# Optimization experiments

Measured on AMD Instinct MI355X. Metric: run time of the kernel, lower is better.

## Reference

```python
import jax, jax.numpy as jnp
import numpy as np

N = 100_000      # nodes
E = 500_000      # edges
D = 128          # node_feature_dim
IN = 2 * D       # VAE in_features
H = 128          # hidden_ch
L = 5            # latent_features
V2 = 3.5
BETA = 10.0


def _init_linear(key, fan_in, fan_out):
    kw, kb = jax.random.split(key)
    bound = 1.0 / np.sqrt(fan_in)
    W = jax.random.uniform(kw, (fan_in, fan_out), jnp.float32, -bound, bound)
    b = jax.random.uniform(kb, (fan_out,), jnp.float32, -bound, bound)
    return W, b


def setup_inputs() -> dict:
    key = jax.random.key(0)
    ks = jax.random.split(key, 12)
    x = jax.random.normal(ks[0], (N, D), jnp.float32)
    row = jax.random.randint(ks[1], (E,), 0, N, jnp.int32)
    col = jax.random.randint(ks[2], (E,), 0, N, jnp.int32)
    eps = jax.random.normal(ks[3], (E, L), jnp.float32)
    # encoder FCBlock: IN -> H -> H -> H -> 2L (ReLU on hidden layers)
    eW0, eb0 = _init_linear(ks[4], IN, H)
    eW1, eb1 = _init_linear(ks[5], H, H)
    eW2, eb2 = _init_linear(ks[6], H, H)
    eW3, eb3 = _init_linear(ks[7], H, 2 * L)
    # decoder FCBlock: L -> H -> H -> H -> IN
    dW0, db0 = _init_linear(ks[8], L, H)
    dW1, db1 = _init_linear(ks[9], H, H)
    dW2, db2 = _init_linear(ks[10], H, H)
    dW3, db3 = _init_linear(ks[11], H, IN)
    return dict(x=x, row=row, col=col, eps=eps,
                eW0=eW0, eb0=eb0, eW1=eW1, eb1=eb1, eW2=eW2, eb2=eb2, eW3=eW3, eb3=eb3,
                dW0=dW0, db0=db0, dW1=dW1, db1=db1, dW2=dW2, db2=db2, dW3=dW3, db3=db3)


def _mlp(h, layers):
    # ReLU on all but the last layer (FCBlock)
    n = len(layers)
    for i, (W, b) in enumerate(layers):
        h = h @ W + b
        if i < n - 1:
            h = jax.nn.relu(h)
    return h


def reference(x, row, col, eps,
              eW0, eb0, eW1, eb1, eW2, eb2, eW3, eb3,
              dW0, db0, dW1, db1, dW2, db2, dW3, db3):
    # gather node pairs -> [E, 2D]
    pair = jnp.concatenate([x[row], x[col]], axis=1)
    enc = _mlp(pair, [(eW0, eb0), (eW1, eb1), (eW2, eb2), (eW3, eb3)])
    mu, logvars = jnp.split(enc, 2, axis=1)          # [E, L] each
    std = jnp.exp(0.5 * logvars)
    z = mu + eps * std                               # reparameterization
    recon = _mlp(z, [(dW0, db0), (dW1, db1), (dW2, db2), (dW3, db3)])
    recon_loss = jnp.sqrt(jnp.sum((recon - pair) ** 2, axis=1))  # [E]
    kl_loss = -0.5 * (1.0 + logvars - mu ** 2 - jnp.exp(logvars)) * BETA  # [E, L]
    edge_affinities = 1.0 / (1.0 + V2 * recon_loss)  # [E]
    return edge_affinities, recon_loss.mean(), kl_loss.mean()
```

## Files before the change

kernel.cpp:

```cpp
#include <hip/hip_runtime.h>
#include <hip/hip_bf16.h>

typedef unsigned short u16;
typedef __attribute__((ext_vector_type(8))) short bf16x8;
typedef __attribute__((ext_vector_type(4))) float f32x4;

#define NE 500000
#define NBLOCKS ((NE + 127) / 128)

#define WE0_U 0u
#define WE1_U 32768u
#define WE2_U 49152u
#define WE3_U 65536u
#define WD0_U 67584u
#define WD1_U 71680u
#define WD2_U 88064u
#define WD3_U 104448u
#define BIAS_F 68608u
#define BE0_F 0
#define BE1_F 128
#define BE2_F 256
#define BE3_F 384
#define BD0_F 400
#define BD1_F 528
#define BD2_F 656
#define BD3_F 784
#define NBIAS 1040
#define ACC_BYTE 278592u

__device__ __forceinline__ u16 f2bf(float f) {
  __hip_bfloat16 h = __float2bfloat16(f);
  u16 u;
  __builtin_memcpy(&u, &h, 2);
  return u;
}

__device__ __forceinline__ f32x4 bcast4(float b) {
  f32x4 v = {b, b, b, b};
  return v;
}

__global__ void prep_kernel(const float* __restrict__ eW0, const float* __restrict__ eb0,
                            const float* __restrict__ eW1, const float* __restrict__ eb1,
                            const float* __restrict__ eW2, const float* __restrict__ eb2,
                            const float* __restrict__ eW3, const float* __restrict__ eb3,
                            const float* __restrict__ dW0, const float* __restrict__ db0,
                            const float* __restrict__ dW1, const float* __restrict__ db1,
                            const float* __restrict__ dW2, const float* __restrict__ db2,
                            const float* __restrict__ dW3, const float* __restrict__ db3,
                            u16* __restrict__ wsu) {
  int t = blockIdx.x * 256 + threadIdx.x;
  float* wsf = (float*)wsu;
  if (t < 32768) {
    int n = t >> 8, k = t & 255;
    wsu[WE0_U + n * 256 + k] = f2bf(eW0[k * 128 + n]);
  } else if (t < 49152) {
    int i = t - 32768, n = i >> 7, k = i & 127;
    wsu[WE1_U + n * 128 + k] = f2bf(eW1[k * 128 + n]);
  } else if (t < 65536) {
    int i = t - 49152, n = i >> 7, k = i & 127;
    wsu[WE2_U + n * 128 + k] = f2bf(eW2[k * 128 + n]);
  } else if (t < 67584) {
    int i = t - 65536, n = i >> 7, k = i & 127;
    wsu[WE3_U + n * 128 + k] = f2bf(n < 10 ? eW3[k * 10 + n] : 0.f);
  } else if (t < 71680) {
    int i = t - 67584, n = i >> 5, k = i & 31;
    wsu[WD0_U + n * 32 + k] = f2bf(k < 5 ? dW0[k * 128 + n] : 0.f);
  } else if (t < 88064) {
    int i = t - 71680, n = i >> 7, k = i & 127;
    wsu[WD1_U + n * 128 + k] = f2bf(dW1[k * 128 + n]);
  } else if (t < 104448) {
    int i = t - 88064, n = i >> 7, k = i & 127;
    wsu[WD2_U + n * 128 + k] = f2bf(dW2[k * 128 + n]);
  } else if (t < 137216) {
    int i = t - 104448, n = i >> 7, k = i & 127;
    wsu[WD3_U + n * 128 + k] = f2bf(dW3[k * 256 + n]);
  } else if (t < 137216 + NBIAS) {
    int i = t - 137216;
    float v;
    if (i < 128) v = eb0[i];
    else if (i < 256) v = eb1[i - 128];
    else if (i < 384) v = eb2[i - 256];
    else if (i < 400) v = (i - 384 < 10) ? eb3[i - 384] : 0.f;
    else if (i < 528) v = db0[i - 400];
    else if (i < 656) v = db1[i - 528];
    else if (i < 784) v = db2[i - 656];
    else v = db3[i - 784];
    wsf[BIAS_F + i] = v;
  } else if (t < 137216 + NBIAS + 2) {
    ((double*)((char*)wsu + ACC_BYTE))[t - 137216 - NBIAS] = 0.0;
  }
}

__device__ __forceinline__ bf16x8 ldA(const u16* buf, int row, int k) {
  int byte = (row * 256 + k * 2) ^ ((row & 7) << 4);
  return *(const bf16x8*)((const char*)buf + byte);
}

__device__ __forceinline__ void init_half(f32x4 acc[2][4], const float* __restrict__ bias,
                                          int nh, int j) {
  #pragma unroll
  for (int n = 0; n < 4; ++n) {
    f32x4 v = bcast4(bias[nh * 64 + n * 16 + j]);
    acc[0][n] = v;
    acc[1][n] = v;
  }
}

template<int LDW>
__device__ __forceinline__ void gemm_half(const u16* __restrict__ inb, const u16* __restrict__ Wt,
                                          int k0, int nh, f32x4 acc[2][4], int rw, int g, int j) {
  #pragma unroll
  for (int kk = 0; kk < 4; ++kk) {
    int k = kk * 32 + g * 8;
    bf16x8 a0 = ldA(inb, rw + j, k);
    bf16x8 a1 = ldA(inb, rw + 16 + j, k);
    #pragma unroll
    for (int n = 0; n < 4; ++n) {
      bf16x8 b = *(const bf16x8*)(Wt + ((nh * 4 + n) * 16 + j) * LDW + k0 + k);
      acc[0][n] = __builtin_amdgcn_mfma_f32_16x16x32_bf16(a0, b, acc[0][n], 0, 0, 0);
      acc[1][n] = __builtin_amdgcn_mfma_f32_16x16x32_bf16(a1, b, acc[1][n], 0, 0, 0);
    }
  }
}

__device__ __forceinline__ void store_half(const f32x4 acc[2][4], u16* outb, int rw, int nh,
                                           int g, int j, bool relu) {
  #pragma unroll
  for (int m = 0; m < 2; ++m)
    #pragma unroll
    for (int n = 0; n < 4; ++n)
      #pragma unroll
      for (int r = 0; r < 4; ++r) {
        float v = acc[m][n][r];
        if (relu) v = fmaxf(v, 0.f);
        int row = rw + m * 16 + g * 4 + r;
        int c = nh * 64 + n * 16 + j;
        int byte = (row * 256 + c * 2) ^ ((row & 7) << 4);
        *(u16*)((char*)outb + byte) = f2bf(v);
      }
}

__device__ __forceinline__ void layer128(const u16* __restrict__ inb, u16* __restrict__ outb,
                                         const u16* __restrict__ Wt, const float* __restrict__ bias,
                                         int rw, int g, int j) {
  #pragma unroll
  for (int nh = 0; nh < 2; ++nh) {
    f32x4 acc[2][4];
    init_half(acc, bias, nh, j);
    gemm_half<128>(inb, Wt, 0, nh, acc, rw, g, j);
    store_half(acc, outb, rw, nh, g, j, true);
  }
}

__device__ __forceinline__ void stage(const float* __restrict__ x, const int* __restrict__ idx,
                                      int e0, u16* buf, int rw, int lane) {
  int rl = rw + (lane >> 1);
  int sub = lane & 1;
  int e = e0 + rl;
  if (e >= NE) e = NE - 1;
  int node = idx[e];
  const f32x4* src = (const f32x4*)(x + (size_t)node * 128 + sub * 64);
  #pragma unroll
  for (int c = 0; c < 8; ++c) {
    f32x4 v0 = src[c * 2];
    f32x4 v1 = src[c * 2 + 1];
    bf16x8 o;
    o[0] = (short)f2bf(v0[0]); o[1] = (short)f2bf(v0[1]);
    o[2] = (short)f2bf(v0[2]); o[3] = (short)f2bf(v0[3]);
    o[4] = (short)f2bf(v1[0]); o[5] = (short)f2bf(v1[1]);
    o[6] = (short)f2bf(v1[2]); o[7] = (short)f2bf(v1[3]);
    int col = sub * 64 + c * 8;
    int byte = (rl * 256 + col * 2) ^ ((rl & 7) << 4);
    *(bf16x8*)((char*)buf + byte) = o;
  }
}

__global__ __launch_bounds__(256, 2) void vae_kernel(
    const float* __restrict__ x, const int* __restrict__ rowi, const int* __restrict__ coli,
    const float* __restrict__ eps, const u16* __restrict__ wsu, double* __restrict__ accg,
    float* __restrict__ out) {
  __shared__ __align__(16) u16 bufA[128 * 128];
  __shared__ __align__(16) u16 bufB[128 * 128];
  __shared__ __align__(16) u16 zbuf[128 * 32];
  __shared__ float redr[4], redk[4];

  const float* wsf = (const float*)wsu;
  const int tid = threadIdx.x;
  const int lane = tid & 63;
  const int wave = tid >> 6;
  const int g = lane >> 4;
  const int j = lane & 15;
  const int rw = wave * 32;
  const int e0 = blockIdx.x * 128;

  {
    bf16x8 zz = {};
    int zr = rw + (lane >> 1);
    int zc = (lane & 1) * 16;
    *(bf16x8*)(zbuf + zr * 32 + zc) = zz;
    *(bf16x8*)(zbuf + zr * 32 + zc + 8) = zz;
  }

  float kl_part = 0.f, rl_part = 0.f;

  stage(x, rowi, e0, bufA, rw, lane);
  stage(x, coli, e0, bufB, rw, lane);

  {
    f32x4 acc8[2][8];
    #pragma unroll
    for (int n = 0; n < 8; ++n) {
      f32x4 v = bcast4(wsf[BIAS_F + BE0_F + n * 16 + j]);
      acc8[0][n] = v;
      acc8[1][n] = v;
    }
    #pragma unroll
    for (int kk = 0; kk < 4; ++kk) {
      int k = kk * 32 + g * 8;
      bf16x8 a0 = ldA(bufA, rw + j, k);
      bf16x8 a1 = ldA(bufA, rw + 16 + j, k);
      #pragma unroll
      for (int n = 0; n < 8; ++n) {
        bf16x8 b = *(const bf16x8*)(wsu + WE0_U + (n * 16 + j) * 256 + k);
        acc8[0][n] = __builtin_amdgcn_mfma_f32_16x16x32_bf16(a0, b, acc8[0][n], 0, 0, 0);
        acc8[1][n] = __builtin_amdgcn_mfma_f32_16x16x32_bf16(a1, b, acc8[1][n], 0, 0, 0);
      }
    }
    #pragma unroll
    for (int kk = 0; kk < 4; ++kk) {
      int k = kk * 32 + g * 8;
      bf16x8 a0 = ldA(bufB, rw + j, k);
      bf16x8 a1 = ldA(bufB, rw + 16 + j, k);
      #pragma unroll
      for (int n = 0; n < 8; ++n) {
        bf16x8 b = *(const bf16x8*)(wsu + WE0_U + (n * 16 + j) * 256 + 128 + k);
        acc8[0][n] = __builtin_amdgcn_mfma_f32_16x16x32_bf16(a0, b, acc8[0][n], 0, 0, 0);
        acc8[1][n] = __builtin_amdgcn_mfma_f32_16x16x32_bf16(a1, b, acc8[1][n], 0, 0, 0);
      }
    }
    #pragma unroll
    for (int m = 0; m < 2; ++m)
      #pragma unroll
      for (int n = 0; n < 8; ++n)
        #pragma unroll
        for (int r = 0; r < 4; ++r) {
          float v = fmaxf(acc8[m][n][r], 0.f);
          int row = rw + m * 16 + g * 4 + r;
          int c = n * 16 + j;
          int byte = (row * 256 + c * 2) ^ ((row & 7) << 4);
          *(u16*)((char*)bufA + byte) = f2bf(v);
        }
  }

  layer128(bufA, bufB, wsu + WE1_U, wsf + BIAS_F + BE1_F, rw, g, j);
  layer128(bufB, bufA, wsu + WE2_U, wsf + BIAS_F + BE2_F, rw, g, j);

  f32x4 a3[2];
  {
    f32x4 v = bcast4(wsf[BIAS_F + BE3_F + j]);
    a3[0] = v;
    a3[1] = v;
    #pragma unroll
    for (int kk = 0; kk < 4; ++kk) {
      int k = kk * 32 + g * 8;
      bf16x8 q0 = ldA(bufA, rw + j, k);
      bf16x8 q1 = ldA(bufA, rw + 16 + j, k);
      bf16x8 b = *(const bf16x8*)(wsu + WE3_U + j * 128 + k);
      a3[0] = __builtin_amdgcn_mfma_f32_16x16x32_bf16(q0, b, a3[0], 0, 0, 0);
      a3[1] = __builtin_amdgcn_mfma_f32_16x16x32_bf16(q1, b, a3[1], 0, 0, 0);
    }
  }

  {
    int src = g * 16 + ((j + 5) & 15);
    #pragma unroll
    for (int m = 0; m < 2; ++m)
      #pragma unroll
      for (int r = 0; r < 4; ++r) {
        float muv = a3[m][r];
        float lvv = __shfl(a3[m][r], src, 64);
        if (j < 5) {
          int row = rw + m * 16 + g * 4 + r;
          int e = e0 + row;
          int ec = e < NE ? e : NE - 1;
          float stdv = __expf(0.5f * lvv);
          float zv = muv + eps[(size_t)ec * 5 + j] * stdv;
          zbuf[row * 32 + j] = f2bf(zv);
          if (e < NE) kl_part += 1.0f + lvv - muv * muv - __expf(lvv);
        }
      }
  }

  #pragma unroll
  for (int nh = 0; nh < 2; ++nh) {
    f32x4 acc[2][4];
    init_half(acc, wsf + BIAS_F + BD0_F, nh, j);
    int k = g * 8;
    bf16x8 q0 = *(const bf16x8*)(zbuf + (rw + j) * 32 + k);
    bf16x8 q1 = *(const bf16x8*)(zbuf + (rw + 16 + j) * 32 + k);
    #pragma unroll
    for (int n = 0; n < 4; ++n) {
      bf16x8 b = *(const bf16x8*)(wsu + WD0_U + ((nh * 4 + n) * 16 + j) * 32 + k);
      acc[0][n] = __builtin_amdgcn_mfma_f32_16x16x32_bf16(q0, b, acc[0][n], 0, 0, 0);
      acc[1][n] = __builtin_amdgcn_mfma_f32_16x16x32_bf16(q1, b, acc[1][n], 0, 0, 0);
    }
    store_half(acc, bufB, rw, nh, g, j, true);
  }

  layer128(bufB, bufA, wsu + WD1_U, wsf + BIAS_F + BD1_F, rw, g, j);
  layer128(bufA, bufB, wsu + WD2_U, wsf + BIAS_F + BD2_F, rw, g, j);

  int rn[2][4], cn[2][4];
  #pragma unroll
  for (int m = 0; m < 2; ++m)
    #pragma unroll
    for (int r = 0; r < 4; ++r) {
      int e = e0 + rw + m * 16 + g * 4 + r;
      int ec = e < NE ? e : NE - 1;
      rn[m][r] = rowi[ec];
      cn[m][r] = coli[ec];
    }

  float rlsq[2][4] = {{0.f, 0.f, 0.f, 0.f}, {0.f, 0.f, 0.f, 0.f}};
  #pragma unroll
  for (int qh = 0; qh < 4; ++qh) {
    f32x4 acc[2][4];
    init_half(acc, wsf + BIAS_F + BD3_F, qh, j);
    gemm_half<128>(bufB, wsu + WD3_U, 0, qh, acc, rw, g, j);
    #pragma unroll
    for (int m = 0; m < 2; ++m)
      #pragma unroll
      for (int n = 0; n < 4; ++n)
        #pragma unroll
        for (int r = 0; r < 4; ++r) {
          int c = qh * 64 + n * 16 + j;
          int node = (c < 128) ? rn[m][r] : cn[m][r];
          float pv = x[(size_t)node * 128 + (c & 127)];
          float d = acc[m][n][r] - pv;
          rlsq[m][r] += d * d;
        }
  }

  #pragma unroll
  for (int m = 0; m < 2; ++m)
    #pragma unroll
    for (int r = 0; r < 4; ++r) {
      float v = rlsq[m][r];
      v += __shfl_xor(v, 1);
      v += __shfl_xor(v, 2);
      v += __shfl_xor(v, 4);
      v += __shfl_xor(v, 8);
      if (j == 0) {
        int e = e0 + rw + m * 16 + g * 4 + r;
        if (e < NE) {
          float rl = sqrtf(v);
          out[e] = 1.0f / (1.0f + 3.5f * rl);
          rl_part += rl;
        }
      }
    }

  float kv = kl_part, rv = rl_part;
  #pragma unroll
  for (int msk = 1; msk < 64; msk <<= 1) {
    kv += __shfl_xor(kv, msk);
    rv += __shfl_xor(rv, msk);
  }
  if (lane == 0) {
    redk[wave] = kv;
    redr[wave] = rv;
  }
  __syncthreads();
  if (tid == 0) {
    atomicAdd(&accg[0], (double)(redr[0] + redr[1] + redr[2] + redr[3]));
    atomicAdd(&accg[1], (double)(redk[0] + redk[1] + redk[2] + redk[3]));
  }
}

__global__ void fin_kernel(const double* __restrict__ accg, float* __restrict__ out) {
  if (threadIdx.x == 0) {
    out[NE] = (float)(accg[0] / (double)NE);
    out[NE + 1] = (float)(accg[1] * (-0.5 * 10.0 / ((double)NE * 5.0)));
  }
}

extern "C" void kernel_launch(void* const* d_in, const int* in_sizes, int n_in,
                              void* d_out, int out_size, void* d_ws, size_t ws_size,
                              hipStream_t stream) {
  (void)in_sizes; (void)n_in; (void)out_size; (void)ws_size;
  const float* x   = (const float*)d_in[0];
  const int*   row = (const int*)d_in[1];
  const int*   col = (const int*)d_in[2];
  const float* eps = (const float*)d_in[3];
  u16* wsu = (u16*)d_ws;
  double* accg = (double*)((char*)d_ws + ACC_BYTE);
  float* out = (float*)d_out;

  prep_kernel<<<541, 256, 0, stream>>>(
      (const float*)d_in[4],  (const float*)d_in[5],  (const float*)d_in[6],  (const float*)d_in[7],
      (const float*)d_in[8],  (const float*)d_in[9],  (const float*)d_in[10], (const float*)d_in[11],
      (const float*)d_in[12], (const float*)d_in[13], (const float*)d_in[14], (const float*)d_in[15],
      (const float*)d_in[16], (const float*)d_in[17], (const float*)d_in[18], (const float*)d_in[19],
      wsu);
  vae_kernel<<<NBLOCKS, 256, 0, stream>>>(x, row, col, eps, wsu, accg, out);
  fin_kernel<<<1, 64, 0, stream>>>(accg, out);
}
```

Measured before the change: 801.6 us.

## Use single in-place LDS buffer with register-held A fragments to cut LDS

Each layer now loads its full A-operand fragments into registers first, then writes its output back into the same LDS tile. This removes the ping-pong second buffer, and the z buffer shrinks from 32 to 8 columns, so LDS use per block drops sharply. The first layer is split into two 64-column halves, with both the row and column inputs preloaded as register fragments. The aim is more resident blocks per CU, at the cost of extra VGPRs for 8–16 held fragments, which may cap occupancy through register pressure instead. Each wave only touches its own 32 rows, so the in-place reuse needs no cross-wave barrier.

```diff
diff --git a/kernel.cpp b/kernel.cpp
--- a/kernel.cpp
+++ b/kernel.cpp
@@ -97,6 +97,15 @@
   return *(const bf16x8*)((const char*)buf + byte);
 }
 
+__device__ __forceinline__ void load_frags(const u16* buf, int rw, int g, int j, bf16x8 f[8]) {
+  #pragma unroll
+  for (int kk = 0; kk < 4; ++kk) {
+    int k = kk * 32 + g * 8;
+    f[kk * 2]     = ldA(buf, rw + j, k);
+    f[kk * 2 + 1] = ldA(buf, rw + 16 + j, k);
+  }
+}
+
 __device__ __forceinline__ void init_half(f32x4 acc[2][4], const float* __restrict__ bias,
                                           int nh, int j) {
   #pragma unroll
@@ -107,19 +116,16 @@
   }
 }
 
-template<int LDW>
-__device__ __forceinline__ void gemm_half(const u16* __restrict__ inb, const u16* __restrict__ Wt,
-                                          int k0, int nh, f32x4 acc[2][4], int rw, int g, int j) {
+__device__ __forceinline__ void gemm_half_f(const bf16x8 f[8], const u16* __restrict__ Wt,
+                                            int nh, f32x4 acc[2][4], int g, int j) {
   #pragma unroll
   for (int kk = 0; kk < 4; ++kk) {
     int k = kk * 32 + g * 8;
-    bf16x8 a0 = ldA(inb, rw + j, k);
-    bf16x8 a1 = ldA(inb, rw + 16 + j, k);
     #pragma unroll
     for (int n = 0; n < 4; ++n) {
-      bf16x8 b = *(const bf16x8*)(Wt + ((nh * 4 + n) * 16 + j) * LDW + k0 + k);
-      acc[0][n] = __builtin_amdgcn_mfma_f32_16x16x32_bf16(a0, b, acc[0][n], 0, 0, 0);
-      acc[1][n] = __builtin_amdgcn_mfma_f32_16x16x32_bf16(a1, b, acc[1][n], 0, 0, 0);
+      bf16x8 b = *(const bf16x8*)(Wt + ((nh * 4 + n) * 16 + j) * 128 + k);
+      acc[0][n] = __builtin_amdgcn_mfma_f32_16x16x32_bf16(f[kk * 2], b, acc[0][n], 0, 0, 0);
+      acc[1][n] = __builtin_amdgcn_mfma_f32_16x16x32_bf16(f[kk * 2 + 1], b, acc[1][n], 0, 0, 0);
     }
   }
 }
@@ -141,15 +147,16 @@
       }
 }
 
-__device__ __forceinline__ void layer128(const u16* __restrict__ inb, u16* __restrict__ outb,
-                                         const u16* __restrict__ Wt, const float* __restrict__ bias,
-                                         int rw, int g, int j) {
+__device__ __forceinline__ void layer_ip(u16* buf, const u16* __restrict__ Wt,
+                                         const float* __restrict__ bias, int rw, int g, int j) {
+  bf16x8 f[8];
+  load_frags(buf, rw, g, j, f);
   #pragma unroll
   for (int nh = 0; nh < 2; ++nh) {
     f32x4 acc[2][4];
     init_half(acc, bias, nh, j);
-    gemm_half<128>(inb, Wt, 0, nh, acc, rw, g, j);
-    store_half(acc, outb, rw, nh, g, j, true);
+    gemm_half_f(f, Wt, nh, acc, g, j);
+    store_half(acc, buf, rw, nh, g, j, true);
   }
 }
 
@@ -180,9 +187,8 @@
     const float* __restrict__ x, const int* __restrict__ rowi, const int* __restrict__ coli,
     const float* __restrict__ eps, const u16* __restrict__ wsu, double* __restrict__ accg,
     float* __restrict__ out) {
-  __shared__ __align__(16) u16 bufA[128 * 128];
-  __shared__ __align__(16) u16 bufB[128 * 128];
-  __shared__ __align__(16) u16 zbuf[128 * 32];
+  __shared__ __align__(16) u16 buf[128 * 128];
+  __shared__ __align__(16) u16 zbuf[128 * 8];
   __shared__ float redr[4], redk[4];
 
   const float* wsf = (const float*)wsu;
@@ -194,81 +200,56 @@
   const int rw = wave * 32;
   const int e0 = blockIdx.x * 128;
 
-  {
+  if (lane < 32) {
     bf16x8 zz = {};
-    int zr = rw + (lane >> 1);
-    int zc = (lane & 1) * 16;
-    *(bf16x8*)(zbuf + zr * 32 + zc) = zz;
-    *(bf16x8*)(zbuf + zr * 32 + zc + 8) = zz;
+    *(bf16x8*)(zbuf + (rw + lane) * 8) = zz;
   }
 
   float kl_part = 0.f, rl_part = 0.f;
 
-  stage(x, rowi, e0, bufA, rw, lane);
-  stage(x, coli, e0, bufB, rw, lane);
-
-  {
-    f32x4 acc8[2][8];
-    #pragma unroll
-    for (int n = 0; n < 8; ++n) {
-      f32x4 v = bcast4(wsf[BIAS_F + BE0_F + n * 16 + j]);
-      acc8[0][n] = v;
-      acc8[1][n] = v;
-    }
+  stage(x, rowi, e0, buf, rw, lane);
+  bf16x8 fA[8];
+  load_frags(buf, rw, g, j, fA);
+  stage(x, coli, e0, buf, rw, lane);
+  bf16x8 fB[8];
+  load_frags(buf, rw, g, j, fB);
+
+  #pragma unroll
+  for (int nh = 0; nh < 2; ++nh) {
+    f32x4 acc[2][4];
+    init_half(acc, wsf + BIAS_F + BE0_F, nh, j);
     #pragma unroll
     for (int kk = 0; kk < 4; ++kk) {
       int k = kk * 32 + g * 8;
-      bf16x8 a0 = ldA(bufA, rw + j, k);
-      bf16x8 a1 = ldA(bufA, rw + 16 + j, k);
-      #pragma unroll
-      for (int n = 0; n < 8; ++n) {
-        bf16x8 b = *(const bf16x8*)(wsu + WE0_U + (n * 16 + j) * 256 + k);
-        acc8[0][n] = __builtin_amdgcn_mfma_f32_16x16x32_bf16(a0, b, acc8[0][n], 0, 0, 0);
-        acc8[1][n] = __builtin_amdgcn_mfma_f32_16x16x32_bf16(a1, b, acc8[1][n], 0, 0, 0);
-      }
-    }
-    #pragma unroll
-    for (int kk = 0; kk < 4; ++kk) {
-      int k = kk * 32 + g * 8;
-      bf16x8 a0 = ldA(bufB, rw + j, k);
-      bf16x8 a1 = ldA(bufB, rw + 16 + j, k);
-      #pragma unroll
-      for (int n = 0; n < 8; ++n) {
-        bf16x8 b = *(const bf16x8*)(wsu + WE0_U + (n * 16 + j) * 256 + 128 + k);
-        acc8[0][n] = __builtin_amdgcn_mfma_f32_16x16x32_bf16(a0, b, acc8[0][n], 0, 0, 0);
-        acc8[1][n] = __builtin_amdgcn_mfma_f32_16x16x32_bf16(a1, b, acc8[1][n], 0, 0, 0);
-      }
-    }
-    #pragma unroll
-    for (int m = 0; m < 2; ++m)
-      #pragma unroll
-      for (int n = 0; n < 8; ++n)
-        #pragma unroll
-        for (int r = 0; r < 4; ++r) {
-          float v = fmaxf(acc8[m][n][r], 0.f);
-          int row = rw + m * 16 + g * 4 + r;
-          int c = n * 16 + j;
-          int byte = (row * 256 + c * 2) ^ ((row & 7) << 4);
-          *(u16*)((char*)bufA + byte) = f2bf(v);
-        }
-  }
-
-  layer128(bufA, bufB, wsu + WE1_U, wsf + BIAS_F + BE1_F, rw, g, j);
-  layer128(bufB, bufA, wsu + WE2_U, wsf + BIAS_F + BE2_F, rw, g, j);
+      #pragma unroll
+      for (int n = 0; n < 4; ++n) {
+        bf16x8 b0 = *(const bf16x8*)(wsu + WE0_U + ((nh * 4 + n) * 16 + j) * 256 + k);
+        bf16x8 b1 = *(const bf16x8*)(wsu + WE0_U + ((nh * 4 + n) * 16 + j) * 256 + 128 + k);
+        acc[0][n] = __builtin_amdgcn_mfma_f32_16x16x32_bf16(fA[kk * 2], b0, acc[0][n], 0, 0, 0);
+        acc[1][n] = __builtin_amdgcn_mfma_f32_16x16x32_bf16(fA[kk * 2 + 1], b0, acc[1][n], 0, 0, 0);
+        acc[0][n] = __builtin_amdgcn_mfma_f32_16x16x32_bf16(fB[kk * 2], b1, acc[0][n], 0, 0, 0);
+        acc[1][n] = __builtin_amdgcn_mfma_f32_16x16x32_bf16(fB[kk * 2 + 1], b1, acc[1][n], 0, 0, 0);
+      }
+    }
+    store_half(acc, buf, rw, nh, g, j, true);
+  }
+
+  layer_ip(buf, wsu + WE1_U, wsf + BIAS_F + BE1_F, rw, g, j);
+  layer_ip(buf, wsu + WE2_U, wsf + BIAS_F + BE2_F, rw, g, j);
 
   f32x4 a3[2];
   {
+    bf16x8 f3[8];
+    load_frags(buf, rw, g, j, f3);
     f32x4 v = bcast4(wsf[BIAS_F + BE3_F + j]);
     a3[0] = v;
     a3[1] = v;
     #pragma unroll
     for (int kk = 0; kk < 4; ++kk) {
       int k = kk * 32 + g * 8;
-      bf16x8 q0 = ldA(bufA, rw + j, k);
-      bf16x8 q1 = ldA(bufA, rw + 16 + j, k);
       bf16x8 b = *(const bf16x8*)(wsu + WE3_U + j * 128 + k);
-      a3[0] = __builtin_amdgcn_mfma_f32_16x16x32_bf16(q0, b, a3[0], 0, 0, 0);
-      a3[1] = __builtin_amdgcn_mfma_f32_16x16x32_bf16(q1, b, a3[1], 0, 0, 0);
+      a3[0] = __builtin_amdgcn_mfma_f32_16x16x32_bf16(f3[kk * 2], b, a3[0], 0, 0, 0);
+      a3[1] = __builtin_amdgcn_mfma_f32_16x16x32_bf16(f3[kk * 2 + 1], b, a3[1], 0, 0, 0);
     }
   }
 
@@ -286,30 +267,35 @@
           int ec = e < NE ? e : NE - 1;
           float stdv = __expf(0.5f * lvv);
           float zv = muv + eps[(size_t)ec * 5 + j] * stdv;
-          zbuf[row * 32 + j] = f2bf(zv);
+          zbuf[row * 8 + j] = f2bf(zv);
           if (e < NE) kl_part += 1.0f + lvv - muv * muv - __expf(lvv);
         }
       }
   }
 
-  #pragma unroll
-  for (int nh = 0; nh < 2; ++nh) {
-    f32x4 acc[2][4];
-    init_half(acc, wsf + BIAS_F + BD0_F, nh, j);
-    int k = g * 8;
-    bf16x8 q0 = *(const bf16x8*)(zbuf + (rw + j) * 32 + k);
-    bf16x8 q1 = *(const bf16x8*)(zbuf + (rw + 16 + j) * 32 + k);
-    #pragma unroll
-    for (int n = 0; n < 4; ++n) {
-      bf16x8 b = *(const bf16x8*)(wsu + WD0_U + ((nh * 4 + n) * 16 + j) * 32 + k);
-      acc[0][n] = __builtin_amdgcn_mfma_f32_16x16x32_bf16(q0, b, acc[0][n], 0, 0, 0);
-      acc[1][n] = __builtin_amdgcn_mfma_f32_16x16x32_bf16(q1, b, acc[1][n], 0, 0, 0);
-    }
-    store_half(acc, bufB, rw, nh, g, j, true);
-  }
-
-  layer128(bufB, bufA, wsu + WD1_U, wsf + BIAS_F + BD1_F, rw, g, j);
-  layer128(bufA, bufB, wsu + WD2_U, wsf + BIAS_F + BD2_F, rw, g, j);
+  {
+    bf16x8 zf0 = {}, zf1 = {};
+    if (g == 0) {
+      zf0 = *(const bf16x8*)(zbuf + (rw + j) * 8);
+      zf1 = *(const bf16x8*)(zbuf + (rw + 16 + j) * 8);
+    }
+    #pragma unroll
+    for (int nh = 0; nh < 2; ++nh) {
+      f32x4 acc[2][4];
+      init_half(acc, wsf + BIAS_F + BD0_F, nh, j);
+      int k = g * 8;
+      #pragma unroll
+      for (int n = 0; n < 4; ++n) {
+        bf16x8 b = *(const bf16x8*)(wsu + WD0_U + ((nh * 4 + n) * 16 + j) * 32 + k);
+        acc[0][n] = __builtin_amdgcn_mfma_f32_16x16x32_bf16(zf0, b, acc[0][n], 0, 0, 0);
+        acc[1][n] = __builtin_amdgcn_mfma_f32_16x16x32_bf16(zf1, b, acc[1][n], 0, 0, 0);
+      }
+      store_half(acc, buf, rw, nh, g, j, true);
+    }
+  }
+
+  layer_ip(buf, wsu + WD1_U, wsf + BIAS_F + BD1_F, rw, g, j);
+  layer_ip(buf, wsu + WD2_U, wsf + BIAS_F + BD2_F, rw, g, j);
 
   int rn[2][4], cn[2][4];
   #pragma unroll
@@ -323,23 +309,27 @@
     }
 
   float rlsq[2][4] = {{0.f, 0.f, 0.f, 0.f}, {0.f, 0.f, 0.f, 0.f}};
-  #pragma unroll
-  for (int qh = 0; qh < 4; ++qh) {
-    f32x4 acc[2][4];
-    init_half(acc, wsf + BIAS_F + BD3_F, qh, j);
-    gemm_half<128>(bufB, wsu + WD3_U, 0, qh, acc, rw, g, j);
-    #pragma unroll
-    for (int m = 0; m < 2; ++m)
-      #pragma unroll
-      for (int n = 0; n < 4; ++n)
+  {
+    bf16x8 f[8];
+    load_frags(buf, rw, g, j, f);
+    #pragma unroll
+    for (int qh = 0; qh < 4; ++qh) {
+      f32x4 acc[2][4];
+      init_half(acc, wsf + BIAS_F + BD3_F, qh, j);
+      gemm_half_f(f, wsu + WD3_U, qh, acc, g, j);
+      #pragma unroll
+      for (int m = 0; m < 2; ++m)
         #pragma unroll
-        for (int r = 0; r < 4; ++r) {
-          int c = qh * 64 + n * 16 + j;
-          int node = (c < 128) ? rn[m][r] : cn[m][r];
-          float pv = x[(size_t)node * 128 + (c & 127)];
-          float d = acc[m][n][r] - pv;
-          rlsq[m][r] += d * d;
-        }
+        for (int n = 0; n < 4; ++n)
+          #pragma unroll
+          for (int r = 0; r < 4; ++r) {
+            int c = qh * 64 + n * 16 + j;
+            int node = (c < 128) ? rn[m][r] : cn[m][r];
+            float pv = x[(size_t)node * 128 + (c & 127)];
+            float d = acc[m][n][r] - pv;
+            rlsq[m][r] += d * d;
+          }
+    }
   }
 
   #pragma unroll
```

After: 769.4 us. 4.0% less time.
